# Kernel optimization log

Hardware: AMD Instinct MI355X
Metric: run time of the kernel (lower is better)

The kernel has to match this reference:

```python
import jax, jax.numpy as jnp
import numpy as np

N_USERS, N_ITEMS, EMB_DIM, N_INTENTS, N_EDGES, N_LAYERS = 50000, 100000, 64, 128, 3000000, 2
N_NODES = N_USERS + N_ITEMS


def _l2norm(x, eps=1e-8):
    # F.normalize(p=2, dim=-1, eps): x / max(||x||, eps)
    n = jnp.sqrt(jnp.sum(x * x, axis=-1, keepdims=True))
    return x / jnp.maximum(n, eps)


def setup_inputs() -> dict:
    key = jax.random.key(0)
    k0, k1, k2, k3, k4, k5 = jax.random.split(key, 6)
    xav_e = np.sqrt(2.0 / (N_NODES + EMB_DIM)).astype(np.float32)
    xav_i = np.sqrt(2.0 / (EMB_DIM + N_INTENTS)).astype(np.float32)
    return {
        "user_emb": jax.random.normal(k0, (N_USERS, EMB_DIM), jnp.float32) * xav_e,
        "item_emb": jax.random.normal(k1, (N_ITEMS, EMB_DIM), jnp.float32) * xav_e,
        "user_intent": jax.random.normal(k2, (EMB_DIM, N_INTENTS), jnp.float32) * xav_i,
        "item_intent": jax.random.normal(k3, (EMB_DIM, N_INTENTS), jnp.float32) * xav_i,
        "all_h": jax.random.randint(k4, (N_EDGES,), 0, N_NODES, jnp.int32),
        "all_t": jax.random.randint(k5, (N_EDGES,), 0, N_NODES, jnp.int32),
    }


def reference(user_emb, item_emb, user_intent, item_intent, all_h, all_t):
    E = all_h.shape[0]

    def spmm(vals, x):
        # y[h] += vals * x[t]  over edges  (torch_sparse.spmm)
        return jax.ops.segment_sum(vals[:, None] * x[all_t], all_h, num_segments=N_NODES)

    # _cal_sparse_adj: G = D^-1/2 A D^-1/2 on the unweighted edge list
    deg = jax.ops.segment_sum(jnp.ones((E,), jnp.float32), all_h, num_segments=N_NODES)
    d_inv_sqrt = jnp.where(deg > 0, deg, 1.0) ** -0.5 * (deg > 0)
    g_values = d_inv_sqrt[all_h] * d_inv_sqrt[all_t]

    def adaptive_values(src):
        # _adaptive_mask: cosine-sim edge weights, row-normalized
        he = _l2norm(src[all_h])
        te = _l2norm(src[all_t])
        edge_alpha = (jnp.sum(he * te, axis=1) + 1.0) * 0.5  # in [0,1]
        row_sum = jax.ops.segment_sum(edge_alpha, all_h, num_segments=N_NODES)
        d_inv = jnp.where(row_sum > 0, 1.0 / jnp.where(row_sum > 0, row_sum, 1.0), 0.0)
        return d_inv[all_h] * edge_alpha

    emb = jnp.concatenate([user_emb, item_emb], axis=0)  # [N, d]
    acc = emb
    for _ in range(N_LAYERS):
        gnn = spmm(g_values, emb)
        u, it = emb[:N_USERS], emb[N_USERS:]
        u_int = jax.nn.softmax(u @ user_intent, axis=1) @ user_intent.T
        i_int = jax.nn.softmax(it @ item_intent, axis=1) @ item_intent.T
        int_e = jnp.concatenate([u_int, i_int], axis=0)
        gaa = spmm(adaptive_values(gnn), emb)
        iaa = spmm(adaptive_values(int_e), emb)
        emb = gnn + int_e + gaa + iaa + emb
        acc = acc + emb
    # torch: sum over stacked layer embeddings == initial + each layer output
    return acc
```

## Files before the change

### kernel.cpp

```cpp
#include <hip/hip_runtime.h>
#include <hip/hip_bf16.h>

#define N_USERS   50000
#define N_ITEMS   100000
#define N_NODES   150000
#define DIM       64
#define N_INTENTS 128
#define N_EDGES   3000000
#define PSHIFT    9
#define PROWS     (1 << PSHIFT)
#define NPART     ((N_NODES + PROWS - 1) >> PSHIFT)
#define CHUNK     16384
#define NCHB      ((N_EDGES + CHUNK - 1) / CHUNK)

typedef __attribute__((ext_vector_type(8))) short short8v;
typedef __attribute__((ext_vector_type(4))) float f32x4;

static __device__ __forceinline__ float wsum64(float v){
#pragma unroll
  for (int m = 32; m >= 1; m >>= 1) v += __shfl_xor(v, m, 64);
  return v;
}
static __device__ __forceinline__ float wmax64(float v){
#pragma unroll
  for (int m = 32; m >= 1; m >>= 1) v = fmaxf(v, __shfl_xor(v, m, 64));
  return v;
}

template<int CTRL>
static __device__ __forceinline__ float dpp_ror_add(float x){
  int t = __builtin_amdgcn_update_dpp(0, __builtin_bit_cast(int, x),
                                      CTRL, 0xF, 0xF, true);
  return x + __builtin_bit_cast(float, t);
}
static __device__ __forceinline__ float row16_allsum(float x){
  x = dpp_ror_add<0x128>(x);
  x = dpp_ror_add<0x124>(x);
  x = dpp_ror_add<0x122>(x);
  x = dpp_ror_add<0x121>(x);
  return x;
}
template<int CTRL>
static __device__ __forceinline__ float dpp_ror_max(float x){
  int t = __builtin_amdgcn_update_dpp(0, __builtin_bit_cast(int, x),
                                      CTRL, 0xF, 0xF, true);
  return fmaxf(x, __builtin_bit_cast(float, t));
}
static __device__ __forceinline__ float row16_allmax(float x){
  x = dpp_ror_max<0x128>(x);
  x = dpp_ror_max<0x124>(x);
  x = dpp_ror_max<0x122>(x);
  x = dpp_ror_max<0x121>(x);
  return x;
}

static __device__ __forceinline__ unsigned short f2bf(float x){
  __hip_bfloat16 h = __float2bfloat16(x);
  return __builtin_bit_cast(unsigned short, h);
}
static __device__ __forceinline__ float bf_lo(unsigned int v){
  return __builtin_bit_cast(float, v << 16);
}
static __device__ __forceinline__ float bf_hi(unsigned int v){
  return __builtin_bit_cast(float, v & 0xFFFF0000u);
}
static __device__ __forceinline__ float bfval(unsigned short h){
  return __builtin_bit_cast(float, (unsigned int)h << 16);
}
static __device__ __forceinline__ void split2(float x, unsigned short& hi,
                                              unsigned short& lo){
  hi = f2bf(x);
  lo = f2bf(x - bfval(hi));
}

__global__ void k_init(const float* __restrict__ ue, const float* __restrict__ ie,
                       float* __restrict__ emb, float* __restrict__ acc,
                       unsigned short* __restrict__ embb){
  int i = blockIdx.x * 256 + threadIdx.x;
  if (i >= N_NODES * DIM) return;
  float v = (i < N_USERS * DIM) ? ue[i] : ie[i - N_USERS * DIM];
  emb[i] = v; acc[i] = v; embb[i] = f2bf(v);
}

__global__ void k_deg(const int* __restrict__ h, int* __restrict__ deg){
  int e = blockIdx.x * 256 + threadIdx.x;
  if (e < N_EDGES) atomicAdd(&deg[h[e]], 1);
}

__global__ void k_scan1(const int* __restrict__ deg, int* __restrict__ tmp,
                        int* __restrict__ aux){
  __shared__ int s[256];
  int t = threadIdx.x, i = blockIdx.x * 256 + t;
  int v = (i < N_NODES) ? deg[i] : 0;
  s[t] = v; __syncthreads();
  for (int off = 1; off < 256; off <<= 1){
    int x = (t >= off) ? s[t - off] : 0;
    __syncthreads();
    s[t] += x;
    __syncthreads();
  }
  if (i < N_NODES) tmp[i] = s[t];
  if (t == 255) aux[blockIdx.x] = s[255];
}

__global__ __launch_bounds__(1024) void k_scan2(int* __restrict__ aux, int n){
  __shared__ int s[1024];
  int t = threadIdx.x;
  int v = (t < n) ? aux[t] : 0;
  s[t] = v; __syncthreads();
  for (int off = 1; off < 1024; off <<= 1){
    int x = (t >= off) ? s[t - off] : 0;
    __syncthreads();
    s[t] += x;
    __syncthreads();
  }
  if (t < n) aux[t] = s[t] - v;
}

__global__ void k_rowptr(const int* __restrict__ tmp, const int* __restrict__ deg,
                         const int* __restrict__ aux, int* __restrict__ rp,
                         float* __restrict__ dis, int* __restrict__ gcur){
  int i = blockIdx.x * 256 + threadIdx.x;
  if (i < N_NODES){
    int v = aux[i >> 8] + tmp[i] - deg[i];
    rp[i] = v;
    int d = deg[i];
    dis[i] = (d > 0) ? (1.f / sqrtf((float)d)) : 0.f;
    if ((i & (PROWS - 1)) == 0) gcur[i >> PSHIFT] = v;
  }
  if (i == 0) rp[N_NODES] = N_EDGES;
}

__global__ __launch_bounds__(256) void k_part1(const int* __restrict__ h,
                                               const int* __restrict__ t,
                                               int* __restrict__ gcur,
                                               unsigned int* __restrict__ stg){
  __shared__ int hist[NPART];
  __shared__ int base[NPART];
  __shared__ int cnt2[NPART];
  int tid = threadIdx.x;
  int s = blockIdx.x * CHUNK;
  int e = min(s + CHUNK, N_EDGES);
  for (int p = tid; p < NPART; p += 256){ hist[p] = 0; cnt2[p] = 0; }
  __syncthreads();
  for (int i = s + tid; i < e; i += 256)
    atomicAdd(&hist[h[i] >> PSHIFT], 1);
  __syncthreads();
  for (int p = tid; p < NPART; p += 256){
    int c = hist[p];
    base[p] = c ? atomicAdd(&gcur[p], c) : 0;
  }
  __syncthreads();
  for (int i = s + tid; i < e; i += 256){
    int hh = h[i];
    int part = hh >> PSHIFT;
    int pos = base[part] + atomicAdd(&cnt2[part], 1);
    stg[pos] = ((unsigned)t[i] << PSHIFT) | (unsigned)(hh & (PROWS - 1));
  }
}

__global__ __launch_bounds__(256) void k_part2(const int* __restrict__ rp,
                                               const unsigned int* __restrict__ stg,
                                               int* __restrict__ t_csr){
  __shared__ int cur[PROWS];
  int b = blockIdx.x, tid = threadIdx.x;
  int row0 = b << PSHIFT;
  int rows = min(PROWS, N_NODES - row0);
  for (int i = tid; i < rows; i += 256) cur[i] = rp[row0 + i];
  __syncthreads();
  int s = rp[row0], e = rp[row0 + rows];
  for (int i = s + tid; i < e; i += 256){
    unsigned int v = stg[i];
    int pos = atomicAdd(&cur[v & (PROWS - 1)], 1);
    t_csr[pos] = (int)(v >> PSHIFT);
  }
}

__global__ void k_spmm_gnn(const int* __restrict__ rp, const int* __restrict__ t_csr,
                           const float* __restrict__ dis,
                           const unsigned short* __restrict__ embb,
                           float* __restrict__ gnn, unsigned short* __restrict__ hgAB){
  int w = (blockIdx.x * 256 + threadIdx.x) >> 6;
  int lane = threadIdx.x & 63;
  if (w >= N_NODES) return;
  int slot = lane >> 3, sub = lane & 7;
  int s = rp[w], e = rp[w + 1];
  float a0=0.f,a1=0.f,a2=0.f,a3=0.f,a4=0.f,a5=0.f,a6=0.f,a7=0.f;
  if (e > s){
    int i = s + slot;
    int t0 = t_csr[min(i, e - 1)];
    int t1 = t_csr[min(i + 8, e - 1)];
    float wt0 = dis[t0];
    uint4 ev0 = *(const uint4*)(embb + (size_t)t0 * 64 + 8 * sub);
    for (; i < e; i += 8){
      int t2 = t_csr[min(i + 16, e - 1)];
      float wt1 = dis[t1];
      uint4 ev1 = *(const uint4*)(embb + (size_t)t1 * 64 + 8 * sub);
      a0 = fmaf(wt0, bf_lo(ev0.x), a0); a1 = fmaf(wt0, bf_hi(ev0.x), a1);
      a2 = fmaf(wt0, bf_lo(ev0.y), a2); a3 = fmaf(wt0, bf_hi(ev0.y), a3);
      a4 = fmaf(wt0, bf_lo(ev0.z), a4); a5 = fmaf(wt0, bf_hi(ev0.z), a5);
      a6 = fmaf(wt0, bf_lo(ev0.w), a6); a7 = fmaf(wt0, bf_hi(ev0.w), a7);
      wt0 = wt1; ev0 = ev1; t1 = t2;
    }
  }
#pragma unroll
  for (int m = 8; m <= 32; m <<= 1){
    a0 += __shfl_xor(a0, m, 64); a1 += __shfl_xor(a1, m, 64);
    a2 += __shfl_xor(a2, m, 64); a3 += __shfl_xor(a3, m, 64);
    a4 += __shfl_xor(a4, m, 64); a5 += __shfl_xor(a5, m, 64);
    a6 += __shfl_xor(a6, m, 64); a7 += __shfl_xor(a7, m, 64);
  }
  float dw = dis[w];
  float g0 = dw*a0, g1 = dw*a1, g2 = dw*a2, g3 = dw*a3;
  float g4 = dw*a4, g5 = dw*a5, g6 = dw*a6, g7 = dw*a7;
  float sq = g0*g0 + g1*g1 + g2*g2 + g3*g3 + g4*g4 + g5*g5 + g6*g6 + g7*g7;
#pragma unroll
  for (int m = 1; m <= 4; m <<= 1) sq += __shfl_xor(sq, m, 64);
  float invn = 1.f / fmaxf(sqrtf(sq), 1e-8f);
  if (slot == 0){
    float4 v0 = make_float4(g0, g1, g2, g3);
    float4 v1 = make_float4(g4, g5, g6, g7);
    ((float4*)gnn)[w * 16 + 2 * sub]     = v0;
    ((float4*)gnn)[w * 16 + 2 * sub + 1] = v1;
    uint4 ob;
    ob.x = (unsigned)f2bf(g0*invn) | ((unsigned)f2bf(g1*invn) << 16);
    ob.y = (unsigned)f2bf(g2*invn) | ((unsigned)f2bf(g3*invn) << 16);
    ob.z = (unsigned)f2bf(g4*invn) | ((unsigned)f2bf(g5*invn) << 16);
    ob.w = (unsigned)f2bf(g6*invn) | ((unsigned)f2bf(g7*invn) << 16);
    *(uint4*)(hgAB + (size_t)w * 128 + 8 * sub) = ob;
  }
}

__global__ void k_wprep(const float* __restrict__ wu, const float* __restrict__ wi,
                        unsigned short* __restrict__ wbuf){
  const float* W = blockIdx.x ? wi : wu;
  unsigned short* seg = wbuf + blockIdx.x * 32768;
  int tid = threadIdx.x;
  for (int i = tid; i < DIM * N_INTENTS; i += 256){
    unsigned short h, l; split2(W[i], h, l);
    seg[16384 + i] = h; seg[24576 + i] = l;
  }
  for (int idx = tid; idx < 16 * 64; idx += 256){
    int f = idx >> 6, lane = idx & 63;
    int nt = f >> 1, ks = f & 1, g = lane >> 4, c = lane & 15;
    int in = 16 * nt + c;
#pragma unroll
    for (int e = 0; e < 8; e++){
      int d = 8 * g + e + 32 * ks;
      unsigned short h, l; split2(W[d * N_INTENTS + in], h, l);
      seg[f * 512 + lane * 8 + e] = h;
      seg[8192 + f * 512 + lane * 8 + e] = l;
    }
  }
}

__global__ __launch_bounds__(256) void k_intent_mfma(
    const unsigned short* __restrict__ wseg, const float* __restrict__ emb,
    unsigned short* __restrict__ out_bf, unsigned short* __restrict__ hgAB,
    int base_node, int count){
  __shared__ __align__(16) unsigned int Pl[4][2048];
  int wid = threadIdx.x >> 6, lane = threadIdx.x & 63;
  int tile = blockIdx.x * 4 + wid;
  if (tile * 16 >= count) return;
  int g = lane >> 4, c = lane & 15;

  const float4* erow = (const float4*)(emb + (size_t)(base_node + tile * 16 + c) * DIM);
  float4 ea0 = erow[2 * g],     eb0 = erow[2 * g + 1];
  float4 ea1 = erow[8 + 2 * g], eb1 = erow[9 + 2 * g];
  short8v ehi[2], elo[2];
  {
    float xs[16] = {ea0.x, ea0.y, ea0.z, ea0.w, eb0.x, eb0.y, eb0.z, eb0.w,
                    ea1.x, ea1.y, ea1.z, ea1.w, eb1.x, eb1.y, eb1.z, eb1.w};
#pragma unroll
    for (int ksi = 0; ksi < 2; ksi++)
#pragma unroll
      for (int e = 0; e < 8; e++){
        unsigned short h, l; split2(xs[ksi * 8 + e], h, l);
        ehi[ksi][e] = (short)h; elo[ksi][e] = (short)l;
      }
  }

  const uint4* w1hi = (const uint4*)wseg;
  const uint4* w1lo = (const uint4*)(wseg + 8192);
  f32x4 acc1[8];
#pragma unroll
  for (int nt = 0; nt < 8; nt++){
    f32x4 a = {0.f, 0.f, 0.f, 0.f};
#pragma unroll
    for (int ks = 0; ks < 2; ks++){
      short8v wh = __builtin_bit_cast(short8v, w1hi[(nt * 2 + ks) * 64 + lane]);
      short8v wl = __builtin_bit_cast(short8v, w1lo[(nt * 2 + ks) * 64 + lane]);
      a = __builtin_amdgcn_mfma_f32_16x16x32_bf16(ehi[ks], wh, a, 0, 0, 0);
      a = __builtin_amdgcn_mfma_f32_16x16x32_bf16(elo[ks], wh, a, 0, 0, 0);
      a = __builtin_amdgcn_mfma_f32_16x16x32_bf16(ehi[ks], wl, a, 0, 0, 0);
    }
    acc1[nt] = a;
  }

  unsigned int* pw = &Pl[wid][0];
#pragma unroll
  for (int r = 0; r < 4; r++){
    float m = acc1[0][r];
#pragma unroll
    for (int nt = 1; nt < 8; nt++) m = fmaxf(m, acc1[nt][r]);
    m = row16_allmax(m);
    float p[8];
    float s = 0.f;
#pragma unroll
    for (int nt = 0; nt < 8; nt++){ p[nt] = __expf(acc1[nt][r] - m); s += p[nt]; }
    s = row16_allsum(s);
    float inv = 1.f / s;
    int node = 4 * g + r;
    int swz = (node & 7) << 2;
    int base = node * 128 + c;
#pragma unroll
    for (int nt = 0; nt < 8; nt++){
      float v = p[nt] * inv;
      unsigned short h, l; split2(v, h, l);
      pw[(base + 16 * nt) ^ swz] = (unsigned int)h | ((unsigned int)l << 16);
    }
  }

  const uint4* pr = (const uint4*)pw;
  short8v phf[4], plf[4];
  int sw = (c & 7) << 2;
#pragma unroll
  for (int ks = 0; ks < 4; ks++){
    int i0 = c * 128 + 8 * g + 32 * ks;
    uint4 ra = pr[(i0 ^ sw) >> 2];
    uint4 rb = pr[((i0 + 4) ^ sw) >> 2];
    unsigned int q[8] = {ra.x, ra.y, ra.z, ra.w, rb.x, rb.y, rb.z, rb.w};
#pragma unroll
    for (int e = 0; e < 8; e++){
      phf[ks][e] = (short)(q[e] & 0xFFFFu);
      plf[ks][e] = (short)(q[e] >> 16);
    }
  }

  const uint4* w2hi = (const uint4*)(wseg + 16384);
  const uint4* w2lo = (const uint4*)(wseg + 24576);
  f32x4 acc2[4];
#pragma unroll
  for (int nt = 0; nt < 4; nt++){
    f32x4 a = {0.f, 0.f, 0.f, 0.f};
#pragma unroll
    for (int ks = 0; ks < 4; ks++){
      int fi = (16 * nt + c) * 16 + ks * 4 + g;
      short8v wh = __builtin_bit_cast(short8v, w2hi[fi]);
      short8v wl = __builtin_bit_cast(short8v, w2lo[fi]);
      a = __builtin_amdgcn_mfma_f32_16x16x32_bf16(phf[ks], wh, a, 0, 0, 0);
      a = __builtin_amdgcn_mfma_f32_16x16x32_bf16(plf[ks], wh, a, 0, 0, 0);
      a = __builtin_amdgcn_mfma_f32_16x16x32_bf16(phf[ks], wl, a, 0, 0, 0);
    }
    acc2[nt] = a;
  }

#pragma unroll
  for (int r = 0; r < 4; r++){
    float sq = 0.f;
#pragma unroll
    for (int nt = 0; nt < 4; nt++) sq = fmaf(acc2[nt][r], acc2[nt][r], sq);
    sq = row16_allsum(sq);
    float invn = 1.f / fmaxf(sqrtf(sq), 1e-8f);
    size_t node = (size_t)(base_node + tile * 16 + 4 * g + r);
    unsigned short* hw = hgAB + node * 128 + 64;
    size_t obase = node * DIM + c;
#pragma unroll
    for (int nt = 0; nt < 4; nt++){
      float v = acc2[nt][r];
      out_bf[obase + 16 * nt] = f2bf(v);
      hw[16 * nt + c] = f2bf(v * invn);
    }
  }
}

__global__ void k_adafuse(const int* __restrict__ rp, const int* __restrict__ t_csr,
                          const unsigned short* __restrict__ hgAB,
                          const uint2* __restrict__ inte_bf2,
                          const unsigned short* __restrict__ embb,
                          const float* __restrict__ emb,
                          float* __restrict__ gnn_io, float* __restrict__ acc,
                          uint2* __restrict__ embb_next2){
  int w = (blockIdx.x * 256 + threadIdx.x) >> 6;
  int lane = threadIdx.x & 63;
  if (w >= N_NODES) return;
  int g = lane >> 4, c = lane & 15;
  const unsigned short* wr = hgAB + (size_t)w * 128;
  short8v bA0 = *(const short8v*)(wr + 8 * g);
  short8v bA1 = *(const short8v*)(wr + 8 * g + 32);
  short8v bB0 = *(const short8v*)(wr + 64 + 8 * g);
  short8v bB1 = *(const short8v*)(wr + 96 + 8 * g);
  int s = rp[w], e = rp[w + 1];
  float4 s1 = make_float4(0.f, 0.f, 0.f, 0.f);
  float4 s2 = make_float4(0.f, 0.f, 0.f, 0.f);
  float r1 = 0.f, r2 = 0.f;
  if (e > s){
    int ia = min(s + c, e - 1);
    int t = t_csr[ia];
    const unsigned short* ra = hgAB + (size_t)t * 128;
    short8v aA0 = *(const short8v*)(ra + 8 * g);
    short8v aA1 = *(const short8v*)(ra + 8 * g + 32);
    short8v aB0 = *(const short8v*)(ra + 64 + 8 * g);
    short8v aB1 = *(const short8v*)(ra + 96 + 8 * g);
    int eb = s + 4 * g;
    uint2 ev0 = *(const uint2*)(embb + (size_t)t_csr[min(eb,     e-1)] * 64 + 4 * c);
    uint2 ev1 = *(const uint2*)(embb + (size_t)t_csr[min(eb + 1, e-1)] * 64 + 4 * c);
    uint2 ev2 = *(const uint2*)(embb + (size_t)t_csr[min(eb + 2, e-1)] * 64 + 4 * c);
    uint2 ev3 = *(const uint2*)(embb + (size_t)t_csr[min(eb + 3, e-1)] * 64 + 4 * c);
    for (int i = s; i < e; i += 16){
      int inx = i + 16;
      int ja = min(inx + c, e - 1);
      int tn = t_csr[ja];
      const unsigned short* rn = hgAB + (size_t)tn * 128;
      short8v nA0 = *(const short8v*)(rn + 8 * g);
      short8v nA1 = *(const short8v*)(rn + 8 * g + 32);
      short8v nB0 = *(const short8v*)(rn + 64 + 8 * g);
      short8v nB1 = *(const short8v*)(rn + 96 + 8 * g);
      int nb = inx + 4 * g;
      uint2 ne0 = *(const uint2*)(embb + (size_t)t_csr[min(nb,     e-1)] * 64 + 4 * c);
      uint2 ne1 = *(const uint2*)(embb + (size_t)t_csr[min(nb + 1, e-1)] * 64 + 4 * c);
      uint2 ne2 = *(const uint2*)(embb + (size_t)t_csr[min(nb + 2, e-1)] * 64 + 4 * c);
      uint2 ne3 = *(const uint2*)(embb + (size_t)t_csr[min(nb + 3, e-1)] * 64 + 4 * c);
      f32x4 p = {0.f, 0.f, 0.f, 0.f};
      f32x4 q = {0.f, 0.f, 0.f, 0.f};
      p = __builtin_amdgcn_mfma_f32_16x16x32_bf16(aA0, bA0, p, 0, 0, 0);
      p = __builtin_amdgcn_mfma_f32_16x16x32_bf16(aA1, bA1, p, 0, 0, 0);
      q = __builtin_amdgcn_mfma_f32_16x16x32_bf16(aB0, bB0, q, 0, 0, 0);
      q = __builtin_amdgcn_mfma_f32_16x16x32_bf16(aB1, bB1, q, 0, 0, 0);
      int ebase = i + 4 * g;
      {
        bool valid = ebase < e;
        float a1v = valid ? fmaf(p[0], 0.5f, 0.5f) : 0.f;
        float a2v = valid ? fmaf(q[0], 0.5f, 0.5f) : 0.f;
        r1 += a1v; r2 += a2v;
        float v0 = bf_lo(ev0.x), v1 = bf_hi(ev0.x), v2 = bf_lo(ev0.y), v3 = bf_hi(ev0.y);
        s1.x = fmaf(a1v, v0, s1.x); s1.y = fmaf(a1v, v1, s1.y);
        s1.z = fmaf(a1v, v2, s1.z); s1.w = fmaf(a1v, v3, s1.w);
        s2.x = fmaf(a2v, v0, s2.x); s2.y = fmaf(a2v, v1, s2.y);
        s2.z = fmaf(a2v, v2, s2.z); s2.w = fmaf(a2v, v3, s2.w);
      }
      {
        bool valid = (ebase + 1) < e;
        float a1v = valid ? fmaf(p[1], 0.5f, 0.5f) : 0.f;
        float a2v = valid ? fmaf(q[1], 0.5f, 0.5f) : 0.f;
        r1 += a1v; r2 += a2v;
        float v0 = bf_lo(ev1.x), v1 = bf_hi(ev1.x), v2 = bf_lo(ev1.y), v3 = bf_hi(ev1.y);
        s1.x = fmaf(a1v, v0, s1.x); s1.y = fmaf(a1v, v1, s1.y);
        s1.z = fmaf(a1v, v2, s1.z); s1.w = fmaf(a1v, v3, s1.w);
        s2.x = fmaf(a2v, v0, s2.x); s2.y = fmaf(a2v, v1, s2.y);
        s2.z = fmaf(a2v, v2, s2.z); s2.w = fmaf(a2v, v3, s2.w);
      }
      {
        bool valid = (ebase + 2) < e;
        float a1v = valid ? fmaf(p[2], 0.5f, 0.5f) : 0.f;
        float a2v = valid ? fmaf(q[2], 0.5f, 0.5f) : 0.f;
        r1 += a1v; r2 += a2v;
        float v0 = bf_lo(ev2.x), v1 = bf_hi(ev2.x), v2 = bf_lo(ev2.y), v3 = bf_hi(ev2.y);
        s1.x = fmaf(a1v, v0, s1.x); s1.y = fmaf(a1v, v1, s1.y);
        s1.z = fmaf(a1v, v2, s1.z); s1.w = fmaf(a1v, v3, s1.w);
        s2.x = fmaf(a2v, v0, s2.x); s2.y = fmaf(a2v, v1, s2.y);
        s2.z = fmaf(a2v, v2, s2.z); s2.w = fmaf(a2v, v3, s2.w);
      }
      {
        bool valid = (ebase + 3) < e;
        float a1v = valid ? fmaf(p[3], 0.5f, 0.5f) : 0.f;
        float a2v = valid ? fmaf(q[3], 0.5f, 0.5f) : 0.f;
        r1 += a1v; r2 += a2v;
        float v0 = bf_lo(ev3.x), v1 = bf_hi(ev3.x), v2 = bf_lo(ev3.y), v3 = bf_hi(ev3.y);
        s1.x = fmaf(a1v, v0, s1.x); s1.y = fmaf(a1v, v1, s1.y);
        s1.z = fmaf(a1v, v2, s1.z); s1.w = fmaf(a1v, v3, s1.w);
        s2.x = fmaf(a2v, v0, s2.x); s2.y = fmaf(a2v, v1, s2.y);
        s2.z = fmaf(a2v, v2, s2.z); s2.w = fmaf(a2v, v3, s2.w);
      }
      aA0 = nA0; aA1 = nA1; aB0 = nB0; aB1 = nB1;
      ev0 = ne0; ev1 = ne1; ev2 = ne2; ev3 = ne3;
    }
  }
#pragma unroll
  for (int m = 16; m <= 32; m <<= 1){
    s1.x += __shfl_xor(s1.x, m, 64); s1.y += __shfl_xor(s1.y, m, 64);
    s1.z += __shfl_xor(s1.z, m, 64); s1.w += __shfl_xor(s1.w, m, 64);
    s2.x += __shfl_xor(s2.x, m, 64); s2.y += __shfl_xor(s2.y, m, 64);
    s2.z += __shfl_xor(s2.z, m, 64); s2.w += __shfl_xor(s2.w, m, 64);
    r1   += __shfl_xor(r1,   m, 64); r2   += __shfl_xor(r2,   m, 64);
  }
  float d1 = (r1 > 0.f) ? 1.f / r1 : 0.f;
  float d2 = (r2 > 0.f) ? 1.f / r2 : 0.f;
  if (g == 0){
    int idx4 = w * 16 + c;
    float4 gg = ((float4*)gnn_io)[idx4];
    uint2 it = inte_bf2[idx4];
    float4 em = ((const float4*)emb)[idx4];
    float4 nv;
    nv.x = gg.x + bf_lo(it.x) + em.x + d1 * s1.x + d2 * s2.x;
    nv.y = gg.y + bf_hi(it.x) + em.y + d1 * s1.y + d2 * s2.y;
    nv.z = gg.z + bf_lo(it.y) + em.z + d1 * s1.z + d2 * s2.z;
    nv.w = gg.w + bf_hi(it.y) + em.w + d1 * s1.w + d2 * s2.w;
    ((float4*)gnn_io)[idx4] = nv;
    float4 ac = ((float4*)acc)[idx4];
    ac.x += nv.x; ac.y += nv.y; ac.z += nv.z; ac.w += nv.w;
    ((float4*)acc)[idx4] = ac;
    uint2 ob;
    ob.x = (unsigned)f2bf(nv.x) | ((unsigned)f2bf(nv.y) << 16);
    ob.y = (unsigned)f2bf(nv.z) | ((unsigned)f2bf(nv.w) << 16);
    embb_next2[idx4] = ob;
  }
}

extern "C" void kernel_launch(void* const* d_in, const int* in_sizes, int n_in,
                              void* d_out, int out_size, void* d_ws, size_t ws_size,
                              hipStream_t stream){
  const float* ue = (const float*)d_in[0];
  const float* ie = (const float*)d_in[1];
  const float* wu = (const float*)d_in[2];
  const float* wi = (const float*)d_in[3];
  const int* all_h = (const int*)d_in[4];
  const int* all_t = (const int*)d_in[5];
  float* acc = (float*)d_out;

  char* p = (char*)d_ws;
  auto take = [&](size_t bytes)->char*{
    char* r = p; p += (bytes + 255) & ~size_t(255); return r;
  };
  float*  embA  = (float*)take(sizeof(float) * N_NODES * DIM);
  float*  embB  = (float*)take(sizeof(float) * N_NODES * DIM);
  unsigned short* hgAB = (unsigned short*)take(sizeof(short) * N_NODES * 128);
  unsigned short* inte_bf = (unsigned short*)take(sizeof(short) * N_NODES * DIM);
  unsigned short* embbA   = (unsigned short*)take(sizeof(short) * N_NODES * DIM);
  unsigned short* embbB   = (unsigned short*)take(sizeof(short) * N_NODES * DIM);
  unsigned short* wbuf    = (unsigned short*)take(sizeof(short) * 2 * 32768);
  int*    t_csr = (int*)take(sizeof(int) * N_EDGES);
  float*  dis   = (float*)take(sizeof(float) * N_NODES);
  int*    deg   = (int*)take(sizeof(int) * N_NODES);
  int*    tmp   = (int*)take(sizeof(int) * N_NODES);
  int*    aux   = (int*)take(sizeof(int) * 1024);
  int*    rp    = (int*)take(sizeof(int) * (N_NODES + 1));
  int*    gcur  = (int*)take(sizeof(int) * NPART);
  if ((size_t)(p - (char*)d_ws) > ws_size) return;
  unsigned int* stg = (unsigned int*)hgAB;

  const int ELEM_B  = (N_NODES * DIM + 255) / 256;
  const int NODEW_B = (N_NODES * 64 + 255) / 256;
  const int EDGE_B  = (N_EDGES + 255) / 256;
  const int NODE_B  = (N_NODES + 255) / 256;

  hipMemsetAsync(deg, 0, sizeof(int) * N_NODES, stream);
  k_init<<<ELEM_B, 256, 0, stream>>>(ue, ie, embA, acc, embbA);
  k_wprep<<<2, 256, 0, stream>>>(wu, wi, wbuf);
  k_deg<<<EDGE_B, 256, 0, stream>>>(all_h, deg);
  k_scan1<<<NODE_B, 256, 0, stream>>>(deg, tmp, aux);
  k_scan2<<<1, 1024, 0, stream>>>(aux, NODE_B);
  k_rowptr<<<NODE_B, 256, 0, stream>>>(tmp, deg, aux, rp, dis, gcur);
  k_part1<<<NCHB, 256, 0, stream>>>(all_h, all_t, gcur, stg);
  k_part2<<<NPART, 256, 0, stream>>>(rp, stg, t_csr);

  const int UT_B = ((N_USERS / 16) + 3) / 4;
  const int IT_B = ((N_ITEMS / 16) + 3) / 4;

  float* eA = embA;
  float* eB = embB;
  unsigned short* ebA = embbA;
  unsigned short* ebB = embbB;
  for (int layer = 0; layer < 2; layer++){
    k_spmm_gnn<<<NODEW_B, 256, 0, stream>>>(rp, t_csr, dis, ebA, eB, hgAB);
    k_intent_mfma<<<UT_B, 256, 0, stream>>>(wbuf, eA, inte_bf, hgAB, 0, N_USERS);
    k_intent_mfma<<<IT_B, 256, 0, stream>>>(wbuf + 32768, eA, inte_bf, hgAB,
                                            N_USERS, N_ITEMS);
    k_adafuse<<<NODEW_B, 256, 0, stream>>>(rp, t_csr, hgAB,
                                           (const uint2*)inte_bf, ebA,
                                           eA, eB, acc, (uint2*)ebB);
    float* t = eA; eA = eB; eB = t;
    unsigned short* tb = ebA; ebA = ebB; ebB = tb;
  }
}
```

Measured before the change: 1.024 ms.

## Fuse GNN SpMM and intent MFMA kernels into one interleaved launch

```diff
diff --git a/kernel.cpp b/kernel.cpp
--- a/kernel.cpp
+++ b/kernel.cpp
@@ -13,17 +13,17 @@
 #define CHUNK     16384
 #define NCHB      ((N_EDGES + CHUNK - 1) / CHUNK)
 
+#define UT_TILES  (N_USERS / 16)
+#define TOT_TILES ((N_USERS + N_ITEMS) / 16)
+#define INT_B     ((TOT_TILES + 3) / 4)
+#define FUSED_G   (17 * INT_B)
+
 typedef __attribute__((ext_vector_type(8))) short short8v;
 typedef __attribute__((ext_vector_type(4))) float f32x4;
 
 static __device__ __forceinline__ float wsum64(float v){
 #pragma unroll
   for (int m = 32; m >= 1; m >>= 1) v += __shfl_xor(v, m, 64);
-  return v;
-}
-static __device__ __forceinline__ float wmax64(float v){
-#pragma unroll
-  for (int m = 32; m >= 1; m >>= 1) v = fmaxf(v, __shfl_xor(v, m, 64));
   return v;
 }
 
@@ -176,61 +176,6 @@
   }
 }
 
-__global__ void k_spmm_gnn(const int* __restrict__ rp, const int* __restrict__ t_csr,
-                           const float* __restrict__ dis,
-                           const unsigned short* __restrict__ embb,
-                           float* __restrict__ gnn, unsigned short* __restrict__ hgAB){
-  int w = (blockIdx.x * 256 + threadIdx.x) >> 6;
-  int lane = threadIdx.x & 63;
-  if (w >= N_NODES) return;
-  int slot = lane >> 3, sub = lane & 7;
-  int s = rp[w], e = rp[w + 1];
-  float a0=0.f,a1=0.f,a2=0.f,a3=0.f,a4=0.f,a5=0.f,a6=0.f,a7=0.f;
-  if (e > s){
-    int i = s + slot;
-    int t0 = t_csr[min(i, e - 1)];
-    int t1 = t_csr[min(i + 8, e - 1)];
-    float wt0 = dis[t0];
-    uint4 ev0 = *(const uint4*)(embb + (size_t)t0 * 64 + 8 * sub);
-    for (; i < e; i += 8){
-      int t2 = t_csr[min(i + 16, e - 1)];
-      float wt1 = dis[t1];
-      uint4 ev1 = *(const uint4*)(embb + (size_t)t1 * 64 + 8 * sub);
-      a0 = fmaf(wt0, bf_lo(ev0.x), a0); a1 = fmaf(wt0, bf_hi(ev0.x), a1);
-      a2 = fmaf(wt0, bf_lo(ev0.y), a2); a3 = fmaf(wt0, bf_hi(ev0.y), a3);
-      a4 = fmaf(wt0, bf_lo(ev0.z), a4); a5 = fmaf(wt0, bf_hi(ev0.z), a5);
-      a6 = fmaf(wt0, bf_lo(ev0.w), a6); a7 = fmaf(wt0, bf_hi(ev0.w), a7);
-      wt0 = wt1; ev0 = ev1; t1 = t2;
-    }
-  }
-#pragma unroll
-  for (int m = 8; m <= 32; m <<= 1){
-    a0 += __shfl_xor(a0, m, 64); a1 += __shfl_xor(a1, m, 64);
-    a2 += __shfl_xor(a2, m, 64); a3 += __shfl_xor(a3, m, 64);
-    a4 += __shfl_xor(a4, m, 64); a5 += __shfl_xor(a5, m, 64);
-    a6 += __shfl_xor(a6, m, 64); a7 += __shfl_xor(a7, m, 64);
-  }
-  float dw = dis[w];
-  float g0 = dw*a0, g1 = dw*a1, g2 = dw*a2, g3 = dw*a3;
-  float g4 = dw*a4, g5 = dw*a5, g6 = dw*a6, g7 = dw*a7;
-  float sq = g0*g0 + g1*g1 + g2*g2 + g3*g3 + g4*g4 + g5*g5 + g6*g6 + g7*g7;
-#pragma unroll
-  for (int m = 1; m <= 4; m <<= 1) sq += __shfl_xor(sq, m, 64);
-  float invn = 1.f / fmaxf(sqrtf(sq), 1e-8f);
-  if (slot == 0){
-    float4 v0 = make_float4(g0, g1, g2, g3);
-    float4 v1 = make_float4(g4, g5, g6, g7);
-    ((float4*)gnn)[w * 16 + 2 * sub]     = v0;
-    ((float4*)gnn)[w * 16 + 2 * sub + 1] = v1;
-    uint4 ob;
-    ob.x = (unsigned)f2bf(g0*invn) | ((unsigned)f2bf(g1*invn) << 16);
-    ob.y = (unsigned)f2bf(g2*invn) | ((unsigned)f2bf(g3*invn) << 16);
-    ob.z = (unsigned)f2bf(g4*invn) | ((unsigned)f2bf(g5*invn) << 16);
-    ob.w = (unsigned)f2bf(g6*invn) | ((unsigned)f2bf(g7*invn) << 16);
-    *(uint4*)(hgAB + (size_t)w * 128 + 8 * sub) = ob;
-  }
-}
-
 __global__ void k_wprep(const float* __restrict__ wu, const float* __restrict__ wi,
                         unsigned short* __restrict__ wbuf){
   const float* W = blockIdx.x ? wi : wu;
@@ -254,122 +199,181 @@
   }
 }
 
-__global__ __launch_bounds__(256) void k_intent_mfma(
-    const unsigned short* __restrict__ wseg, const float* __restrict__ emb,
-    unsigned short* __restrict__ out_bf, unsigned short* __restrict__ hgAB,
-    int base_node, int count){
+__global__ __launch_bounds__(256) void k_gnn_intent(
+    const int* __restrict__ rp, const int* __restrict__ t_csr,
+    const float* __restrict__ dis, const unsigned short* __restrict__ embb,
+    const float* __restrict__ emb, const unsigned short* __restrict__ wbuf,
+    float* __restrict__ gnn, unsigned short* __restrict__ hgAB,
+    unsigned short* __restrict__ out_bf){
   __shared__ __align__(16) unsigned int Pl[4][2048];
+  int bid = blockIdx.x;
   int wid = threadIdx.x >> 6, lane = threadIdx.x & 63;
-  int tile = blockIdx.x * 4 + wid;
-  if (tile * 16 >= count) return;
-  int g = lane >> 4, c = lane & 15;
-
-  const float4* erow = (const float4*)(emb + (size_t)(base_node + tile * 16 + c) * DIM);
-  float4 ea0 = erow[2 * g],     eb0 = erow[2 * g + 1];
-  float4 ea1 = erow[8 + 2 * g], eb1 = erow[9 + 2 * g];
-  short8v ehi[2], elo[2];
-  {
-    float xs[16] = {ea0.x, ea0.y, ea0.z, ea0.w, eb0.x, eb0.y, eb0.z, eb0.w,
-                    ea1.x, ea1.y, ea1.z, ea1.w, eb1.x, eb1.y, eb1.z, eb1.w};
-#pragma unroll
-    for (int ksi = 0; ksi < 2; ksi++)
+
+  if ((bid % 17) == 16){
+    int gt = (bid / 17) * 4 + wid;
+    if (gt >= TOT_TILES) return;
+    int node0; const unsigned short* wseg;
+    if (gt < UT_TILES){ node0 = gt * 16;                       wseg = wbuf; }
+    else              { node0 = N_USERS + (gt - UT_TILES) * 16; wseg = wbuf + 32768; }
+    int g = lane >> 4, c = lane & 15;
+
+    const float4* erow = (const float4*)(emb + (size_t)(node0 + c) * DIM);
+    float4 ea0 = erow[2 * g],     eb0 = erow[2 * g + 1];
+    float4 ea1 = erow[8 + 2 * g], eb1 = erow[9 + 2 * g];
+    short8v ehi[2], elo[2];
+    {
+      float xs[16] = {ea0.x, ea0.y, ea0.z, ea0.w, eb0.x, eb0.y, eb0.z, eb0.w,
+                      ea1.x, ea1.y, ea1.z, ea1.w, eb1.x, eb1.y, eb1.z, eb1.w};
+#pragma unroll
+      for (int ksi = 0; ksi < 2; ksi++)
+#pragma unroll
+        for (int e = 0; e < 8; e++){
+          unsigned short h, l; split2(xs[ksi * 8 + e], h, l);
+          ehi[ksi][e] = (short)h; elo[ksi][e] = (short)l;
+        }
+    }
+
+    const uint4* w1hi = (const uint4*)wseg;
+    const uint4* w1lo = (const uint4*)(wseg + 8192);
+    f32x4 acc1[8];
+#pragma unroll
+    for (int nt = 0; nt < 8; nt++){
+      f32x4 a = {0.f, 0.f, 0.f, 0.f};
+#pragma unroll
+      for (int ks = 0; ks < 2; ks++){
+        short8v wh = __builtin_bit_cast(short8v, w1hi[(nt * 2 + ks) * 64 + lane]);
+        short8v wl = __builtin_bit_cast(short8v, w1lo[(nt * 2 + ks) * 64 + lane]);
+        a = __builtin_amdgcn_mfma_f32_16x16x32_bf16(ehi[ks], wh, a, 0, 0, 0);
+        a = __builtin_amdgcn_mfma_f32_16x16x32_bf16(elo[ks], wh, a, 0, 0, 0);
+        a = __builtin_amdgcn_mfma_f32_16x16x32_bf16(ehi[ks], wl, a, 0, 0, 0);
+      }
+      acc1[nt] = a;
+    }
+
+    unsigned int* pw = &Pl[wid][0];
+#pragma unroll
+    for (int r = 0; r < 4; r++){
+      float m = acc1[0][r];
+#pragma unroll
+      for (int nt = 1; nt < 8; nt++) m = fmaxf(m, acc1[nt][r]);
+      m = row16_allmax(m);
+      float p[8];
+      float s = 0.f;
+#pragma unroll
+      for (int nt = 0; nt < 8; nt++){ p[nt] = __expf(acc1[nt][r] - m); s += p[nt]; }
+      s = row16_allsum(s);
+      float inv = 1.f / s;
+      int node = 4 * g + r;
+      int swz = (node & 7) << 2;
+      int base = node * 128 + c;
+#pragma unroll
+      for (int nt = 0; nt < 8; nt++){
+        float v = p[nt] * inv;
+        unsigned short h, l; split2(v, h, l);
+        pw[(base + 16 * nt) ^ swz] = (unsigned int)h | ((unsigned int)l << 16);
+      }
+    }
+
+    const uint4* pr = (const uint4*)pw;
+    short8v phf[4], plf[4];
+    int sw = (c & 7) << 2;
+#pragma unroll
+    for (int ks = 0; ks < 4; ks++){
+      int i0 = c * 128 + 8 * g + 32 * ks;
+      uint4 ra = pr[(i0 ^ sw) >> 2];
+      uint4 rb = pr[((i0 + 4) ^ sw) >> 2];
+      unsigned int q[8] = {ra.x, ra.y, ra.z, ra.w, rb.x, rb.y, rb.z, rb.w};
 #pragma unroll
       for (int e = 0; e < 8; e++){
-        unsigned short h, l; split2(xs[ksi * 8 + e], h, l);
-        ehi[ksi][e] = (short)h; elo[ksi][e] = (short)l;
+        phf[ks][e] = (short)(q[e] & 0xFFFFu);
+        plf[ks][e] = (short)(q[e] >> 16);
       }
-  }
-
-  const uint4* w1hi = (const uint4*)wseg;
-  const uint4* w1lo = (const uint4*)(wseg + 8192);
-  f32x4 acc1[8];
-#pragma unroll
-  for (int nt = 0; nt < 8; nt++){
-    f32x4 a = {0.f, 0.f, 0.f, 0.f};
-#pragma unroll
-    for (int ks = 0; ks < 2; ks++){
-      short8v wh = __builtin_bit_cast(short8v, w1hi[(nt * 2 + ks) * 64 + lane]);
-      short8v wl = __builtin_bit_cast(short8v, w1lo[(nt * 2 + ks) * 64 + lane]);
-      a = __builtin_amdgcn_mfma_f32_16x16x32_bf16(ehi[ks], wh, a, 0, 0, 0);
-      a = __builtin_amdgcn_mfma_f32_16x16x32_bf16(elo[ks], wh, a, 0, 0, 0);
-      a = __builtin_amdgcn_mfma_f32_16x16x32_bf16(ehi[ks], wl, a, 0, 0, 0);
-    }
-    acc1[nt] = a;
-  }
-
-  unsigned int* pw = &Pl[wid][0];
-#pragma unroll
-  for (int r = 0; r < 4; r++){
-    float m = acc1[0][r];
-#pragma unroll
-    for (int nt = 1; nt < 8; nt++) m = fmaxf(m, acc1[nt][r]);
-    m = row16_allmax(m);
-    float p[8];
-    float s = 0.f;
-#pragma unroll
-    for (int nt = 0; nt < 8; nt++){ p[nt] = __expf(acc1[nt][r] - m); s += p[nt]; }
-    s = row16_allsum(s);
-    float inv = 1.f / s;
-    int node = 4 * g + r;
-    int swz = (node & 7) << 2;
-    int base = node * 128 + c;
-#pragma unroll
-    for (int nt = 0; nt < 8; nt++){
-      float v = p[nt] * inv;
-      unsigned short h, l; split2(v, h, l);
-      pw[(base + 16 * nt) ^ swz] = (unsigned int)h | ((unsigned int)l << 16);
-    }
-  }
-
-  const uint4* pr = (const uint4*)pw;
-  short8v phf[4], plf[4];
-  int sw = (c & 7) << 2;
-#pragma unroll
-  for (int ks = 0; ks < 4; ks++){
-    int i0 = c * 128 + 8 * g + 32 * ks;
-    uint4 ra = pr[(i0 ^ sw) >> 2];
-    uint4 rb = pr[((i0 + 4) ^ sw) >> 2];
-    unsigned int q[8] = {ra.x, ra.y, ra.z, ra.w, rb.x, rb.y, rb.z, rb.w};
-#pragma unroll
-    for (int e = 0; e < 8; e++){
-      phf[ks][e] = (short)(q[e] & 0xFFFFu);
-      plf[ks][e] = (short)(q[e] >> 16);
-    }
-  }
-
-  const uint4* w2hi = (const uint4*)(wseg + 16384);
-  const uint4* w2lo = (const uint4*)(wseg + 24576);
-  f32x4 acc2[4];
-#pragma unroll
-  for (int nt = 0; nt < 4; nt++){
-    f32x4 a = {0.f, 0.f, 0.f, 0.f};
-#pragma unroll
-    for (int ks = 0; ks < 4; ks++){
-      int fi = (16 * nt + c) * 16 + ks * 4 + g;
-      short8v wh = __builtin_bit_cast(short8v, w2hi[fi]);
-      short8v wl = __builtin_bit_cast(short8v, w2lo[fi]);
-      a = __builtin_amdgcn_mfma_f32_16x16x32_bf16(phf[ks], wh, a, 0, 0, 0);
-      a = __builtin_amdgcn_mfma_f32_16x16x32_bf16(plf[ks], wh, a, 0, 0, 0);
-      a = __builtin_amdgcn_mfma_f32_16x16x32_bf16(phf[ks], wl, a, 0, 0, 0);
-    }
-    acc2[nt] = a;
-  }
-
-#pragma unroll
-  for (int r = 0; r < 4; r++){
-    float sq = 0.f;
-#pragma unroll
-    for (int nt = 0; nt < 4; nt++) sq = fmaf(acc2[nt][r], acc2[nt][r], sq);
-    sq = row16_allsum(sq);
+    }
+
+    const uint4* w2hi = (const uint4*)(wseg + 16384);
+    const uint4* w2lo = (const uint4*)(wseg + 24576);
+    f32x4 acc2[4];
+#pragma unroll
+    for (int nt = 0; nt < 4; nt++){
+      f32x4 a = {0.f, 0.f, 0.f, 0.f};
+#pragma unroll
+      for (int ks = 0; ks < 4; ks++){
+        int fi = (16 * nt + c) * 16 + ks * 4 + g;
+        short8v wh = __builtin_bit_cast(short8v, w2hi[fi]);
+        short8v wl = __builtin_bit_cast(short8v, w2lo[fi]);
+        a = __builtin_amdgcn_mfma_f32_16x16x32_bf16(phf[ks], wh, a, 0, 0, 0);
+        a = __builtin_amdgcn_mfma_f32_16x16x32_bf16(plf[ks], wh, a, 0, 0, 0);
+        a = __builtin_amdgcn_mfma_f32_16x16x32_bf16(phf[ks], wl, a, 0, 0, 0);
+      }
+      acc2[nt] = a;
+    }
+
+#pragma unroll
+    for (int r = 0; r < 4; r++){
+      float sq = 0.f;
+#pragma unroll
+      for (int nt = 0; nt < 4; nt++) sq = fmaf(acc2[nt][r], acc2[nt][r], sq);
+      sq = row16_allsum(sq);
+      float invn = 1.f / fmaxf(sqrtf(sq), 1e-8f);
+      size_t node = (size_t)(node0 + 4 * g + r);
+      unsigned short* hw = hgAB + node * 128 + 64;
+      size_t obase = node * DIM + c;
+#pragma unroll
+      for (int nt = 0; nt < 4; nt++){
+        float v = acc2[nt][r];
+        out_bf[obase + 16 * nt] = f2bf(v);
+        hw[16 * nt + c] = f2bf(v * invn);
+      }
+    }
+  } else {
+    int sidx = bid - bid / 17;
+    int w = sidx * 4 + wid;
+    if (w >= N_NODES) return;
+    int slot = lane >> 3, sub = lane & 7;
+    int s = rp[w], e = rp[w + 1];
+    float a0=0.f,a1=0.f,a2=0.f,a3=0.f,a4=0.f,a5=0.f,a6=0.f,a7=0.f;
+    if (e > s){
+      int i = s + slot;
+      int t0 = t_csr[min(i, e - 1)];
+      int t1 = t_csr[min(i + 8, e - 1)];
+      float wt0 = dis[t0];
+      uint4 ev0 = *(const uint4*)(embb + (size_t)t0 * 64 + 8 * sub);
+      for (; i < e; i += 8){
+        int t2 = t_csr[min(i + 16, e - 1)];
+        float wt1 = dis[t1];
+        uint4 ev1 = *(const uint4*)(embb + (size_t)t1 * 64 + 8 * sub);
+        a0 = fmaf(wt0, bf_lo(ev0.x), a0); a1 = fmaf(wt0, bf_hi(ev0.x), a1);
+        a2 = fmaf(wt0, bf_lo(ev0.y), a2); a3 = fmaf(wt0, bf_hi(ev0.y), a3);
+        a4 = fmaf(wt0, bf_lo(ev0.z), a4); a5 = fmaf(wt0, bf_hi(ev0.z), a5);
+        a6 = fmaf(wt0, bf_lo(ev0.w), a6); a7 = fmaf(wt0, bf_hi(ev0.w), a7);
+        wt0 = wt1; ev0 = ev1; t1 = t2;
+      }
+    }
+#pragma unroll
+    for (int m = 8; m <= 32; m <<= 1){
+      a0 += __shfl_xor(a0, m, 64); a1 += __shfl_xor(a1, m, 64);
+      a2 += __shfl_xor(a2, m, 64); a3 += __shfl_xor(a3, m, 64);
+      a4 += __shfl_xor(a4, m, 64); a5 += __shfl_xor(a5, m, 64);
+      a6 += __shfl_xor(a6, m, 64); a7 += __shfl_xor(a7, m, 64);
+    }
+    float dw = dis[w];
+    float g0 = dw*a0, g1 = dw*a1, g2 = dw*a2, g3 = dw*a3;
+    float g4 = dw*a4, g5 = dw*a5, g6 = dw*a6, g7 = dw*a7;
+    float sq = g0*g0 + g1*g1 + g2*g2 + g3*g3 + g4*g4 + g5*g5 + g6*g6 + g7*g7;
+#pragma unroll
+    for (int m = 1; m <= 4; m <<= 1) sq += __shfl_xor(sq, m, 64);
     float invn = 1.f / fmaxf(sqrtf(sq), 1e-8f);
-    size_t node = (size_t)(base_node + tile * 16 + 4 * g + r);
-    unsigned short* hw = hgAB + node * 128 + 64;
-    size_t obase = node * DIM + c;
-#pragma unroll
-    for (int nt = 0; nt < 4; nt++){
-      float v = acc2[nt][r];
-      out_bf[obase + 16 * nt] = f2bf(v);
-      hw[16 * nt + c] = f2bf(v * invn);
+    if (slot == 0){
+      float4 v0 = make_float4(g0, g1, g2, g3);
+      float4 v1 = make_float4(g4, g5, g6, g7);
+      ((float4*)gnn)[w * 16 + 2 * sub]     = v0;
+      ((float4*)gnn)[w * 16 + 2 * sub + 1] = v1;
+      uint4 ob;
+      ob.x = (unsigned)f2bf(g0*invn) | ((unsigned)f2bf(g1*invn) << 16);
+      ob.y = (unsigned)f2bf(g2*invn) | ((unsigned)f2bf(g3*invn) << 16);
+      ob.z = (unsigned)f2bf(g4*invn) | ((unsigned)f2bf(g5*invn) << 16);
+      ob.w = (unsigned)f2bf(g6*invn) | ((unsigned)f2bf(g7*invn) << 16);
+      *(uint4*)(hgAB + (size_t)w * 128 + 8 * sub) = ob;
     }
   }
 }
@@ -394,87 +398,94 @@
   float4 s1 = make_float4(0.f, 0.f, 0.f, 0.f);
   float4 s2 = make_float4(0.f, 0.f, 0.f, 0.f);
   float r1 = 0.f, r2 = 0.f;
-  if (e > s){
-    int ia = min(s + c, e - 1);
+
+  auto loadA = [&](int i, short8v& A0, short8v& A1, short8v& B0, short8v& B1){
+    int ia = min(i + c, e - 1);
     int t = t_csr[ia];
     const unsigned short* ra = hgAB + (size_t)t * 128;
-    short8v aA0 = *(const short8v*)(ra + 8 * g);
-    short8v aA1 = *(const short8v*)(ra + 8 * g + 32);
-    short8v aB0 = *(const short8v*)(ra + 64 + 8 * g);
-    short8v aB1 = *(const short8v*)(ra + 96 + 8 * g);
-    int eb = s + 4 * g;
-    uint2 ev0 = *(const uint2*)(embb + (size_t)t_csr[min(eb,     e-1)] * 64 + 4 * c);
-    uint2 ev1 = *(const uint2*)(embb + (size_t)t_csr[min(eb + 1, e-1)] * 64 + 4 * c);
-    uint2 ev2 = *(const uint2*)(embb + (size_t)t_csr[min(eb + 2, e-1)] * 64 + 4 * c);
-    uint2 ev3 = *(const uint2*)(embb + (size_t)t_csr[min(eb + 3, e-1)] * 64 + 4 * c);
-    for (int i = s; i < e; i += 16){
-      int inx = i + 16;
-      int ja = min(inx + c, e - 1);
-      int tn = t_csr[ja];
-      const unsigned short* rn = hgAB + (size_t)tn * 128;
-      short8v nA0 = *(const short8v*)(rn + 8 * g);
-      short8v nA1 = *(const short8v*)(rn + 8 * g + 32);
-      short8v nB0 = *(const short8v*)(rn + 64 + 8 * g);
-      short8v nB1 = *(const short8v*)(rn + 96 + 8 * g);
-      int nb = inx + 4 * g;
-      uint2 ne0 = *(const uint2*)(embb + (size_t)t_csr[min(nb,     e-1)] * 64 + 4 * c);
-      uint2 ne1 = *(const uint2*)(embb + (size_t)t_csr[min(nb + 1, e-1)] * 64 + 4 * c);
-      uint2 ne2 = *(const uint2*)(embb + (size_t)t_csr[min(nb + 2, e-1)] * 64 + 4 * c);
-      uint2 ne3 = *(const uint2*)(embb + (size_t)t_csr[min(nb + 3, e-1)] * 64 + 4 * c);
-      f32x4 p = {0.f, 0.f, 0.f, 0.f};
-      f32x4 q = {0.f, 0.f, 0.f, 0.f};
-      p = __builtin_amdgcn_mfma_f32_16x16x32_bf16(aA0, bA0, p, 0, 0, 0);
-      p = __builtin_amdgcn_mfma_f32_16x16x32_bf16(aA1, bA1, p, 0, 0, 0);
-      q = __builtin_amdgcn_mfma_f32_16x16x32_bf16(aB0, bB0, q, 0, 0, 0);
-      q = __builtin_amdgcn_mfma_f32_16x16x32_bf16(aB1, bB1, q, 0, 0, 0);
-      int ebase = i + 4 * g;
-      {
-        bool valid = ebase < e;
-        float a1v = valid ? fmaf(p[0], 0.5f, 0.5f) : 0.f;
-        float a2v = valid ? fmaf(q[0], 0.5f, 0.5f) : 0.f;
-        r1 += a1v; r2 += a2v;
-        float v0 = bf_lo(ev0.x), v1 = bf_hi(ev0.x), v2 = bf_lo(ev0.y), v3 = bf_hi(ev0.y);
-        s1.x = fmaf(a1v, v0, s1.x); s1.y = fmaf(a1v, v1, s1.y);
-        s1.z = fmaf(a1v, v2, s1.z); s1.w = fmaf(a1v, v3, s1.w);
-        s2.x = fmaf(a2v, v0, s2.x); s2.y = fmaf(a2v, v1, s2.y);
-        s2.z = fmaf(a2v, v2, s2.z); s2.w = fmaf(a2v, v3, s2.w);
-      }
-      {
-        bool valid = (ebase + 1) < e;
-        float a1v = valid ? fmaf(p[1], 0.5f, 0.5f) : 0.f;
-        float a2v = valid ? fmaf(q[1], 0.5f, 0.5f) : 0.f;
-        r1 += a1v; r2 += a2v;
-        float v0 = bf_lo(ev1.x), v1 = bf_hi(ev1.x), v2 = bf_lo(ev1.y), v3 = bf_hi(ev1.y);
-        s1.x = fmaf(a1v, v0, s1.x); s1.y = fmaf(a1v, v1, s1.y);
-        s1.z = fmaf(a1v, v2, s1.z); s1.w = fmaf(a1v, v3, s1.w);
-        s2.x = fmaf(a2v, v0, s2.x); s2.y = fmaf(a2v, v1, s2.y);
-        s2.z = fmaf(a2v, v2, s2.z); s2.w = fmaf(a2v, v3, s2.w);
-      }
-      {
-        bool valid = (ebase + 2) < e;
-        float a1v = valid ? fmaf(p[2], 0.5f, 0.5f) : 0.f;
-        float a2v = valid ? fmaf(q[2], 0.5f, 0.5f) : 0.f;
-        r1 += a1v; r2 += a2v;
-        float v0 = bf_lo(ev2.x), v1 = bf_hi(ev2.x), v2 = bf_lo(ev2.y), v3 = bf_hi(ev2.y);
-        s1.x = fmaf(a1v, v0, s1.x); s1.y = fmaf(a1v, v1, s1.y);
-        s1.z = fmaf(a1v, v2, s1.z); s1.w = fmaf(a1v, v3, s1.w);
-        s2.x = fmaf(a2v, v0, s2.x); s2.y = fmaf(a2v, v1, s2.y);
-        s2.z = fmaf(a2v, v2, s2.z); s2.w = fmaf(a2v, v3, s2.w);
-      }
-      {
-        bool valid = (ebase + 3) < e;
-        float a1v = valid ? fmaf(p[3], 0.5f, 0.5f) : 0.f;
-        float a2v = valid ? fmaf(q[3], 0.5f, 0.5f) : 0.f;
-        r1 += a1v; r2 += a2v;
-        float v0 = bf_lo(ev3.x), v1 = bf_hi(ev3.x), v2 = bf_lo(ev3.y), v3 = bf_hi(ev3.y);
-        s1.x = fmaf(a1v, v0, s1.x); s1.y = fmaf(a1v, v1, s1.y);
-        s1.z = fmaf(a1v, v2, s1.z); s1.w = fmaf(a1v, v3, s1.w);
-        s2.x = fmaf(a2v, v0, s2.x); s2.y = fmaf(a2v, v1, s2.y);
-        s2.z = fmaf(a2v, v2, s2.z); s2.w = fmaf(a2v, v3, s2.w);
-      }
+    A0 = *(const short8v*)(ra + 8 * g);
+    A1 = *(const short8v*)(ra + 8 * g + 32);
+    B0 = *(const short8v*)(ra + 64 + 8 * g);
+    B1 = *(const short8v*)(ra + 96 + 8 * g);
+  };
+  auto loadE = [&](int i, uint2& E0, uint2& E1, uint2& E2, uint2& E3){
+    int eb = i + 4 * g;
+    E0 = *(const uint2*)(embb + (size_t)t_csr[min(eb,     e-1)] * 64 + 4 * c);
+    E1 = *(const uint2*)(embb + (size_t)t_csr[min(eb + 1, e-1)] * 64 + 4 * c);
+    E2 = *(const uint2*)(embb + (size_t)t_csr[min(eb + 2, e-1)] * 64 + 4 * c);
+    E3 = *(const uint2*)(embb + (size_t)t_csr[min(eb + 3, e-1)] * 64 + 4 * c);
+  };
+  auto body = [&](int i, short8v aA0, short8v aA1, short8v aB0, short8v aB1,
+                  uint2 ev0, uint2 ev1, uint2 ev2, uint2 ev3){
+    f32x4 p = {0.f, 0.f, 0.f, 0.f};
+    f32x4 q = {0.f, 0.f, 0.f, 0.f};
+    p = __builtin_amdgcn_mfma_f32_16x16x32_bf16(aA0, bA0, p, 0, 0, 0);
+    p = __builtin_amdgcn_mfma_f32_16x16x32_bf16(aA1, bA1, p, 0, 0, 0);
+    q = __builtin_amdgcn_mfma_f32_16x16x32_bf16(aB0, bB0, q, 0, 0, 0);
+    q = __builtin_amdgcn_mfma_f32_16x16x32_bf16(aB1, bB1, q, 0, 0, 0);
+    int ebase = i + 4 * g;
+    {
+      bool valid = ebase < e;
+      float a1v = valid ? fmaf(p[0], 0.5f, 0.5f) : 0.f;
+      float a2v = valid ? fmaf(q[0], 0.5f, 0.5f) : 0.f;
+      r1 += a1v; r2 += a2v;
+      float v0 = bf_lo(ev0.x), v1 = bf_hi(ev0.x), v2 = bf_lo(ev0.y), v3 = bf_hi(ev0.y);
+      s1.x = fmaf(a1v, v0, s1.x); s1.y = fmaf(a1v, v1, s1.y);
+      s1.z = fmaf(a1v, v2, s1.z); s1.w = fmaf(a1v, v3, s1.w);
+      s2.x = fmaf(a2v, v0, s2.x); s2.y = fmaf(a2v, v1, s2.y);
+      s2.z = fmaf(a2v, v2, s2.z); s2.w = fmaf(a2v, v3, s2.w);
+    }
+    {
+      bool valid = (ebase + 1) < e;
+      float a1v = valid ? fmaf(p[1], 0.5f, 0.5f) : 0.f;
+      float a2v = valid ? fmaf(q[1], 0.5f, 0.5f) : 0.f;
+      r1 += a1v; r2 += a2v;
+      float v0 = bf_lo(ev1.x), v1 = bf_hi(ev1.x), v2 = bf_lo(ev1.y), v3 = bf_hi(ev1.y);
+      s1.x = fmaf(a1v, v0, s1.x); s1.y = fmaf(a1v, v1, s1.y);
+      s1.z = fmaf(a1v, v2, s1.z); s1.w = fmaf(a1v, v3, s1.w);
+      s2.x = fmaf(a2v, v0, s2.x); s2.y = fmaf(a2v, v1, s2.y);
+      s2.z = fmaf(a2v, v2, s2.z); s2.w = fmaf(a2v, v3, s2.w);
+    }
+    {
+      bool valid = (ebase + 2) < e;
+      float a1v = valid ? fmaf(p[2], 0.5f, 0.5f) : 0.f;
+      float a2v = valid ? fmaf(q[2], 0.5f, 0.5f) : 0.f;
+      r1 += a1v; r2 += a2v;
+      float v0 = bf_lo(ev2.x), v1 = bf_hi(ev2.x), v2 = bf_lo(ev2.y), v3 = bf_hi(ev2.y);
+      s1.x = fmaf(a1v, v0, s1.x); s1.y = fmaf(a1v, v1, s1.y);
+      s1.z = fmaf(a1v, v2, s1.z); s1.w = fmaf(a1v, v3, s1.w);
+      s2.x = fmaf(a2v, v0, s2.x); s2.y = fmaf(a2v, v1, s2.y);
+      s2.z = fmaf(a2v, v2, s2.z); s2.w = fmaf(a2v, v3, s2.w);
+    }
+    {
+      bool valid = (ebase + 3) < e;
+      float a1v = valid ? fmaf(p[3], 0.5f, 0.5f) : 0.f;
+      float a2v = valid ? fmaf(q[3], 0.5f, 0.5f) : 0.f;
+      r1 += a1v; r2 += a2v;
+      float v0 = bf_lo(ev3.x), v1 = bf_hi(ev3.x), v2 = bf_lo(ev3.y), v3 = bf_hi(ev3.y);
+      s1.x = fmaf(a1v, v0, s1.x); s1.y = fmaf(a1v, v1, s1.y);
+      s1.z = fmaf(a1v, v2, s1.z); s1.w = fmaf(a1v, v3, s1.w);
+      s2.x = fmaf(a2v, v0, s2.x); s2.y = fmaf(a2v, v1, s2.y);
+      s2.z = fmaf(a2v, v2, s2.z); s2.w = fmaf(a2v, v3, s2.w);
+    }
+  };
+
+  if (e > s){
+    short8v aA0, aA1, aB0, aB1;
+    uint2 ev0, ev1, ev2, ev3;
+    loadA(s, aA0, aA1, aB0, aB1);
+    loadE(s, ev0, ev1, ev2, ev3);
+    int i = s;
+    for (; i + 16 < e; i += 16){
+      short8v nA0, nA1, nB0, nB1;
+      uint2 ne0, ne1, ne2, ne3;
+      loadA(i + 16, nA0, nA1, nB0, nB1);
+      loadE(i + 16, ne0, ne1, ne2, ne3);
+      body(i, aA0, aA1, aB0, aB1, ev0, ev1, ev2, ev3);
       aA0 = nA0; aA1 = nA1; aB0 = nB0; aB1 = nB1;
       ev0 = ne0; ev1 = ne1; ev2 = ne2; ev3 = ne3;
     }
+    body(i, aA0, aA1, aB0, aB1, ev0, ev1, ev2, ev3);
   }
 #pragma unroll
   for (int m = 16; m <= 32; m <<= 1){
@@ -554,18 +565,13 @@
   k_part1<<<NCHB, 256, 0, stream>>>(all_h, all_t, gcur, stg);
   k_part2<<<NPART, 256, 0, stream>>>(rp, stg, t_csr);
 
-  const int UT_B = ((N_USERS / 16) + 3) / 4;
-  const int IT_B = ((N_ITEMS / 16) + 3) / 4;
-
   float* eA = embA;
   float* eB = embB;
   unsigned short* ebA = embbA;
   unsigned short* ebB = embbB;
   for (int layer = 0; layer < 2; layer++){
-    k_spmm_gnn<<<NODEW_B, 256, 0, stream>>>(rp, t_csr, dis, ebA, eB, hgAB);
-    k_intent_mfma<<<UT_B, 256, 0, stream>>>(wbuf, eA, inte_bf, hgAB, 0, N_USERS);
-    k_intent_mfma<<<IT_B, 256, 0, stream>>>(wbuf + 32768, eA, inte_bf, hgAB,
-                                            N_USERS, N_ITEMS);
+    k_gnn_intent<<<FUSED_G, 256, 0, stream>>>(rp, t_csr, dis, ebA, eA, wbuf,
+                                              eB, hgAB, inte_bf);
     k_adafuse<<<NODEW_B, 256, 0, stream>>>(rp, t_csr, hgAB,
                                            (const uint2*)inte_bf, ebA,
                                            eA, eB, acc, (uint2*)ebB);
```

After: 1.094 ms. 1.07x slower.
